# Kernel optimization log

Measured on AMD Instinct MI355X. Metric: run time of the kernel, lower is better.

Reference implementation:

```python
import jax, jax.numpy as jnp
import numpy as np


def _euclidean_cdist(x, q):
    # torch.cdist with p=2: pairwise L2 distances, shape [B, Q]
    x2 = jnp.sum(x * x, axis=-1, keepdims=True)          # [B, 1]
    q2 = jnp.sum(q * q, axis=-1)[None, :]                # [1, Q]
    d2 = x2 + q2 - 2.0 * (x @ q.T)                        # [B, Q]
    return jnp.sqrt(jnp.maximum(d2, 0.0))


def setup_inputs() -> dict:
    key = jax.random.key(0)
    k1, k2 = jax.random.split(key)
    x = jax.random.normal(k1, (1024, 256), dtype=jnp.float32)
    queue = jax.random.normal(k2, (32768, 256), dtype=jnp.float32)
    return {"x": x, "queue": queue}


def reference(x, queue):
    # Queue update: concat then keep the newest max_size rows (queue assumed full)
    max_size = queue.shape[0]
    q = jnp.concatenate([queue, x], axis=0)[-max_size:]   # [Q, F]
    # Distance matrix + top-2 nearest (topk of negated distances)
    d = _euclidean_cdist(x, q)                            # [B, Q]
    _, idx = jax.lax.top_k(-d, 2)                         # [B, 2]
    # Second-nearest neighbor (first is the point itself, dist 0)
    return q[idx[:, 1]]                                   # [B, F]
```

## Files before the change

kernel.cpp:

```cpp
#include <hip/hip_runtime.h>
#include <stdint.h>

#define B_ROWS 1024
#define FEAT   256
#define QSZ    32768
#define SHIFT  1024
#define QX     (QSZ - B_ROWS)
#define NQB    256
#define NXB    8
#define MARGIN 8.0f

typedef float  v4f __attribute__((ext_vector_type(4)));
typedef short  v8s __attribute__((ext_vector_type(8)));

__device__ __forceinline__ uint32_t key_flip(uint32_t u) {
    return u ^ ((uint32_t)((int32_t)u >> 31) | 0x80000000u);
}
__device__ __forceinline__ float key_m(uint32_t k) {
    uint32_t u = k & 0xFFFF8000u;
    u = (u & 0x80000000u) ? (u ^ 0x80000000u) : ~u;
    return __uint_as_float(u);
}
__device__ __forceinline__ void k2_insert(uint32_t& k1, uint32_t& k2, uint32_t key) {
    uint32_t hi = max(k1, key); k1 = min(k1, key); k2 = min(k2, hi);
}
__device__ __forceinline__ uint2 k2_merge(uint2 a, uint2 b) {
    uint32_t hi = max(a.x, b.x);
    uint2 r; r.x = min(a.x, b.x); r.y = min(min(a.y, b.y), hi);
    return r;
}

struct Top2 { float m1; int j1; float m2; int j2; };
__device__ __forceinline__ bool better(float ma, int ja, float mb, int jb) {
    return (ma < mb) || (ma == mb && ja < jb);
}
__device__ __forceinline__ void t2_insert(Top2& t, float m, int j) {
    if (better(m, j, t.m1, t.j1)) { t.m2 = t.m1; t.j2 = t.j1; t.m1 = m; t.j1 = j; }
    else if (better(m, j, t.m2, t.j2)) { t.m2 = m; t.j2 = j; }
}

__device__ __forceinline__ const float* q_row_ptr(int j, const float* x, const float* queue) {
    return (j < QX) ? (queue + (size_t)(j + SHIFT) * FEAT) : (x + (size_t)(j - QX) * FEAT);
}

__device__ __forceinline__ unsigned short f2bf(float f) {
    uint32_t u = __float_as_uint(f);
    uint32_t r = u + 0x7FFFu + ((u >> 16) & 1u);
    return (unsigned short)(r >> 16);
}

__device__ __forceinline__ void lds_load16(const void* g, void* l) {
    __builtin_amdgcn_global_load_lds(
        (const __attribute__((address_space(1))) uint32_t*)g,
        (__attribute__((address_space(3))) uint32_t*)l, 16, 0, 0);
}

__global__ __launch_bounds__(256) void convert_kernel(const float* __restrict__ x,
                                                      const float* __restrict__ queue,
                                                      unsigned short* __restrict__ q_bf,
                                                      float* __restrict__ q2) {
    int wave = threadIdx.x >> 6, lane = threadIdx.x & 63;
    int j = blockIdx.x * 4 + wave;
    const float4* row = (const float4*)q_row_ptr(j, x, queue);
    float4 v = row[lane];
    float s = v.x * v.x + v.y * v.y + v.z * v.z + v.w * v.w;
#pragma unroll
    for (int off = 32; off; off >>= 1) s += __shfl_xor(s, off, 64);
    if (lane == 0) q2[j] = s;
    ushort4 h;
    h.x = f2bf(v.x); h.y = f2bf(v.y); h.z = f2bf(v.z); h.w = f2bf(v.w);
    ((ushort4*)q_bf)[(size_t)j * 64 + lane] = h;
}

__global__ __launch_bounds__(256, 3) void nn_mfma(const unsigned short* __restrict__ q_bf,
                                                  const float* __restrict__ q2,
                                                  uint2* __restrict__ partials) {
    __shared__ unsigned short As[128 * 64];
    __shared__ unsigned short Bs[128 * 64];
    __shared__ float sq2[128];
    __shared__ uint2 scr[128][2];

    const int t    = threadIdx.x;
    const int w    = t >> 6, lane = t & 63;
    const int wm   = w >> 1, wn = w & 1;
    const int quad = lane >> 4, l16 = lane & 15;
    const int gy   = blockIdx.x;
    const int gx   = blockIdx.y;

    const unsigned short* x_bf = q_bf + (size_t)QX * FEAT;

    if (t < 128) sq2[t] = q2[gy * 128 + t];

    v4f acc[4][4];
#pragma unroll
    for (int a = 0; a < 4; ++a)
#pragma unroll
        for (int b = 0; b < 4; ++b) acc[a][b] = (v4f)0.0f;

    const int srow = lane >> 3;
    const int sg   = (lane & 7) ^ srow;

    for (int c = 0; c < 4; ++c) {
        __syncthreads();
#pragma unroll
        for (int kk = 0; kk < 4; ++kk) {
            int row = w * 32 + kk * 8 + srow;
            const unsigned short* ga = q_bf + (size_t)(gy * 128 + row) * FEAT + c * 64 + sg * 8;
            const unsigned short* gb = x_bf + (size_t)(gx * 128 + row) * FEAT + c * 64 + sg * 8;
            lds_load16(ga, &As[(w * 32 + kk * 8) * 64]);
            lds_load16(gb, &Bs[(w * 32 + kk * 8) * 64]);
        }
        __syncthreads();
#pragma unroll
        for (int ks = 0; ks < 2; ++ks) {
            v8s fa[4], fb[4];
            const int goff  = (((ks * 4 + quad) ^ (l16 & 7)) << 4);
            const int abase = (wm * 64 + l16) * 128 + goff;
            const int bbase = (wn * 64 + l16) * 128 + goff;
#pragma unroll
            for (int tm = 0; tm < 4; ++tm)
                fa[tm] = *(const v8s*)((const char*)As + abase + tm * 2048);
#pragma unroll
            for (int tn = 0; tn < 4; ++tn)
                fb[tn] = *(const v8s*)((const char*)Bs + bbase + tn * 2048);
#pragma unroll
            for (int tm = 0; tm < 4; ++tm)
#pragma unroll
                for (int tn = 0; tn < 4; ++tn)
                    acc[tm][tn] = __builtin_amdgcn_mfma_f32_16x16x32_bf16(fa[tm], fb[tn], acc[tm][tn], 0, 0, 0);
        }
    }

    float q2r[4][4];
#pragma unroll
    for (int tm = 0; tm < 4; ++tm) {
        v4f qq = *(const v4f*)&sq2[wm * 64 + tm * 16 + quad * 4];
#pragma unroll
        for (int r = 0; r < 4; ++r) q2r[tm][r] = qq[r];
    }
    const int jbase = gy * 128 + wm * 64 + quad * 4;

    uint2 best[4];
#pragma unroll
    for (int tn = 0; tn < 4; ++tn) {
        uint32_t k1 = 0xFFFFFFFFu, k2 = 0xFFFFFFFFu;
#pragma unroll
        for (int tm = 0; tm < 4; ++tm)
#pragma unroll
            for (int r = 0; r < 4; ++r) {
                float m = fmaf(-2.0f, acc[tm][tn][r], q2r[tm][r]);
                uint32_t u = key_flip(__float_as_uint(m));
                uint32_t key = (u & 0xFFFF8000u) | (uint32_t)(jbase + tm * 16 + r);
                k2_insert(k1, k2, key);
            }
#pragma unroll
        for (int mask = 16; mask <= 32; mask <<= 1) {
            uint32_t o1 = __shfl_xor(k1, mask, 64);
            uint32_t o2 = __shfl_xor(k2, mask, 64);
            uint32_t hi = max(k1, o1);
            k1 = min(k1, o1);
            k2 = min(min(k2, o2), hi);
        }
        best[tn] = make_uint2(k1, k2);
    }
    if (quad == 0) {
#pragma unroll
        for (int tn = 0; tn < 4; ++tn) scr[wn * 64 + tn * 16 + l16][wm] = best[tn];
    }
    __syncthreads();
    if (t < 128) {
        uint2 r = k2_merge(scr[t][0], scr[t][1]);
        partials[(size_t)(gx * 128 + t) * NQB + gy] = r;
    }
}

__global__ __launch_bounds__(256) void nn_finalize(const float* __restrict__ x,
                                                   const float* __restrict__ queue,
                                                   const float* __restrict__ q2,
                                                   const uint2* __restrict__ partials,
                                                   float* __restrict__ out) {
    __shared__ float    xs[256];
    __shared__ uint2    red[256];
    __shared__ int      list[64];
    __shared__ float    escore[64];
    __shared__ int      s_cnt;
    __shared__ uint32_t s_kcut;
    __shared__ int      s_j2;

    const int t = threadIdx.x, i = blockIdx.x;
    const int w = t >> 6, lane = t & 63;

    xs[t] = x[(size_t)i * FEAT + t];
    uint2 p = partials[(size_t)i * NQB + t];
    red[t] = p;
    if (t == 0) s_cnt = 0;
    __syncthreads();

    if (w == 0) {
        uint2 a = red[lane];
        a = k2_merge(a, red[lane + 64]);
        a = k2_merge(a, red[lane + 128]);
        a = k2_merge(a, red[lane + 192]);
#pragma unroll
        for (int mask = 1; mask <= 32; mask <<= 1) {
            uint2 o;
            o.x = __shfl_xor(a.x, mask, 64);
            o.y = __shfl_xor(a.y, mask, 64);
            a = k2_merge(a, o);
        }
        if (lane == 0) {
            float cutf = key_m(a.y) + MARGIN;
            s_kcut = key_flip(__float_as_uint(cutf)) | 0x7FFFu;
        }
    }
    __syncthreads();
    uint32_t kcut = s_kcut;
    if (p.x <= kcut) { int q_ = atomicAdd(&s_cnt, 1); if (q_ < 64) list[q_] = (int)(p.x & 0x7FFFu); }
    if (p.y <= kcut) { int q_ = atomicAdd(&s_cnt, 1); if (q_ < 64) list[q_] = (int)(p.y & 0x7FFFu); }
    __syncthreads();
    int n = min(s_cnt, 64);

    for (int c = w; c < n; c += 4) {
        int j = list[c];
        const float4* qr = (const float4*)q_row_ptr(j, x, queue);
        float4 qv = qr[lane];
        float4 xv = ((const float4*)xs)[lane];
        float s = qv.x * xv.x + qv.y * xv.y + qv.z * xv.z + qv.w * xv.w;
#pragma unroll
        for (int off = 32; off; off >>= 1) s += __shfl_xor(s, off, 64);
        if (lane == 0) escore[c] = q2[j] - 2.0f * s;
    }
    __syncthreads();
    if (t == 0) {
        Top2 a;
        a.m1 = __builtin_inff(); a.j1 = 0x7FFFFFFF;
        a.m2 = __builtin_inff(); a.j2 = 0x7FFFFFFF;
        for (int c = 0; c < n; ++c) t2_insert(a, escore[c], list[c]);
        s_j2 = a.j2;
    }
    __syncthreads();
    out[(size_t)i * FEAT + t] = q_row_ptr(s_j2, x, queue)[t];
}

extern "C" void kernel_launch(void* const* d_in, const int* in_sizes, int n_in,
                              void* d_out, int out_size, void* d_ws, size_t ws_size,
                              hipStream_t stream) {
    const float* x     = (const float*)d_in[0];
    const float* queue = (const float*)d_in[1];

    unsigned short* q_bf     = (unsigned short*)d_ws;
    float*          q2       = (float*)((char*)d_ws + (16u << 20));
    uint2*          partials = (uint2*)((char*)d_ws + (17u << 20));

    convert_kernel<<<QSZ / 4, 256, 0, stream>>>(x, queue, q_bf, q2);
    nn_mfma<<<dim3(NQB, NXB), 256, 0, stream>>>(q_bf, q2, partials);
    nn_finalize<<<B_ROWS, 256, 0, stream>>>(x, queue, q2, partials, (float*)d_out);
}
```

Before: 112.8 us.

## Double-buffer LDS staging in MFMA kernel and remap block order for L2 reuse

Splits the K loop into eight 32-wide chunks with two LDS buffers, so global-to-LDS loads for the next chunk are issued before the MFMAs on the current one. Synchronisation uses explicit vmcnt waits, and setprio raises priority around the MFMA block. The 2D grid becomes a 1D grid with a swizzled mapping that groups blocks sharing q rows, aiming for better cache reuse. It also reads q2 directly from global memory instead of staging it in shared memory. The cost is more barriers per chunk and a hand-tuned waitcnt that must match the number of issued loads.

```diff
diff --git a/kernel.cpp b/kernel.cpp
--- a/kernel.cpp
+++ b/kernel.cpp
@@ -72,24 +72,37 @@
     ((ushort4*)q_bf)[(size_t)j * 64 + lane] = h;
 }
 
+__device__ __forceinline__ void stage_chunk(const unsigned short* gA, const unsigned short* gB,
+                                            unsigned short* asb, unsigned short* bsb,
+                                            int w, int c) {
+    lds_load16(gA + (size_t)c * 32,             asb + (w * 32) * 32);
+    lds_load16(gA + (size_t)c * 32 + 16 * FEAT, asb + (w * 32 + 16) * 32);
+    lds_load16(gB + (size_t)c * 32,             bsb + (w * 32) * 32);
+    lds_load16(gB + (size_t)c * 32 + 16 * FEAT, bsb + (w * 32 + 16) * 32);
+}
+
 __global__ __launch_bounds__(256, 3) void nn_mfma(const unsigned short* __restrict__ q_bf,
                                                   const float* __restrict__ q2,
                                                   uint2* __restrict__ partials) {
-    __shared__ unsigned short As[128 * 64];
-    __shared__ unsigned short Bs[128 * 64];
-    __shared__ float sq2[128];
+    __shared__ unsigned short As[2][128 * 32];
+    __shared__ unsigned short Bs[2][128 * 32];
     __shared__ uint2 scr[128][2];
 
     const int t    = threadIdx.x;
     const int w    = t >> 6, lane = t & 63;
     const int wm   = w >> 1, wn = w & 1;
     const int quad = lane >> 4, l16 = lane & 15;
-    const int gy   = blockIdx.x;
-    const int gx   = blockIdx.y;
+
+    const int p  = blockIdx.x;
+    const int gy = (p & 7) * 32 + (p >> 6);
+    const int gx = (p >> 3) & 7;
 
     const unsigned short* x_bf = q_bf + (size_t)QX * FEAT;
 
-    if (t < 128) sq2[t] = q2[gy * 128 + t];
+    const int srow = lane >> 2;
+    const int sgl  = (lane & 3) ^ ((lane >> 3) & 3);
+    const unsigned short* gA = q_bf + (size_t)(gy * 128 + w * 32 + srow) * FEAT + sgl * 8;
+    const unsigned short* gB = x_bf + (size_t)(gx * 128 + w * 32 + srow) * FEAT + sgl * 8;
 
     v4f acc[4][4];
 #pragma unroll
@@ -97,44 +110,41 @@
 #pragma unroll
         for (int b = 0; b < 4; ++b) acc[a][b] = (v4f)0.0f;
 
-    const int srow = lane >> 3;
-    const int sg   = (lane & 7) ^ srow;
-
-    for (int c = 0; c < 4; ++c) {
-        __syncthreads();
-#pragma unroll
-        for (int kk = 0; kk < 4; ++kk) {
-            int row = w * 32 + kk * 8 + srow;
-            const unsigned short* ga = q_bf + (size_t)(gy * 128 + row) * FEAT + c * 64 + sg * 8;
-            const unsigned short* gb = x_bf + (size_t)(gx * 128 + row) * FEAT + c * 64 + sg * 8;
-            lds_load16(ga, &As[(w * 32 + kk * 8) * 64]);
-            lds_load16(gb, &Bs[(w * 32 + kk * 8) * 64]);
-        }
-        __syncthreads();
-#pragma unroll
-        for (int ks = 0; ks < 2; ++ks) {
-            v8s fa[4], fb[4];
-            const int goff  = (((ks * 4 + quad) ^ (l16 & 7)) << 4);
-            const int abase = (wm * 64 + l16) * 128 + goff;
-            const int bbase = (wn * 64 + l16) * 128 + goff;
-#pragma unroll
-            for (int tm = 0; tm < 4; ++tm)
-                fa[tm] = *(const v8s*)((const char*)As + abase + tm * 2048);
+    const int gphys = quad ^ ((l16 >> 1) & 3);
+    const char* Ard = (const char*)&As[0][0] + (size_t)(wm * 64 + l16) * 64 + gphys * 16;
+    const char* Brd = (const char*)&Bs[0][0] + (size_t)(wn * 64 + l16) * 64 + gphys * 16;
+
+    stage_chunk(gA, gB, As[0], Bs[0], w, 0);
+
+#pragma unroll
+    for (int c = 0; c < 8; ++c) {
+        if (c < 7) stage_chunk(gA, gB, As[(c + 1) & 1], Bs[(c + 1) & 1], w, c + 1);
+        __builtin_amdgcn_sched_barrier(0);
+        if (c < 7) asm volatile("s_waitcnt vmcnt(4)" ::: "memory");
+        else       asm volatile("s_waitcnt vmcnt(0)" ::: "memory");
+        __builtin_amdgcn_s_barrier();
+
+        const char* Ac = Ard + (c & 1) * 8192;
+        const char* Bc = Brd + (c & 1) * 8192;
+        v8s fa[4], fb[4];
+#pragma unroll
+        for (int tm = 0; tm < 4; ++tm) fa[tm] = *(const v8s*)(Ac + tm * 1024);
+#pragma unroll
+        for (int tn = 0; tn < 4; ++tn) fb[tn] = *(const v8s*)(Bc + tn * 1024);
+        __builtin_amdgcn_s_setprio(1);
+#pragma unroll
+        for (int tm = 0; tm < 4; ++tm)
 #pragma unroll
             for (int tn = 0; tn < 4; ++tn)
-                fb[tn] = *(const v8s*)((const char*)Bs + bbase + tn * 2048);
-#pragma unroll
-            for (int tm = 0; tm < 4; ++tm)
-#pragma unroll
-                for (int tn = 0; tn < 4; ++tn)
-                    acc[tm][tn] = __builtin_amdgcn_mfma_f32_16x16x32_bf16(fa[tm], fb[tn], acc[tm][tn], 0, 0, 0);
-        }
+                acc[tm][tn] = __builtin_amdgcn_mfma_f32_16x16x32_bf16(fa[tm], fb[tn], acc[tm][tn], 0, 0, 0);
+        __builtin_amdgcn_s_setprio(0);
+        __builtin_amdgcn_s_barrier();
     }
 
     float q2r[4][4];
 #pragma unroll
     for (int tm = 0; tm < 4; ++tm) {
-        v4f qq = *(const v4f*)&sq2[wm * 64 + tm * 16 + quad * 4];
+        v4f qq = *(const v4f*)(q2 + gy * 128 + wm * 64 + tm * 16 + quad * 4);
 #pragma unroll
         for (int r = 0; r < 4; ++r) q2r[tm][r] = qq[r];
     }
@@ -253,6 +263,6 @@
     uint2*          partials = (uint2*)((char*)d_ws + (17u << 20));
 
     convert_kernel<<<QSZ / 4, 256, 0, stream>>>(x, queue, q_bf, q2);
-    nn_mfma<<<dim3(NQB, NXB), 256, 0, stream>>>(q_bf, q2, partials);
+    nn_mfma<<<NQB * NXB, 256, 0, stream>>>(q_bf, q2, partials);
     nn_finalize<<<B_ROWS, 256, 0, stream>>>(x, queue, q2, partials, (float*)d_out);
 }
```

Measured after the change: 111.4 us, median of 2. About the same (-1.2%).
